# Optimization experiments

Measured on AMD Instinct MI355X. Metric: run time of the kernel, lower is better.

Reference implementation:

```python
import jax, jax.numpy as jnp
import numpy as np

IN_FEATURES = 4096
OUT_FEATURES = 8192
LUT_SIZE = 65536  # 256 * 256 two-level codebook


def setup_inputs() -> dict:
    key = jax.random.key(0)
    k_x, k_b, k_f, k_s, k_l = jax.random.split(key, 5)
    x = jax.random.normal(k_x, (2, 256, IN_FEATURES), dtype=jnp.float32)
    base_idx = jax.random.randint(k_b, (OUT_FEATURES, IN_FEATURES), 0, 256, dtype=jnp.int32)
    fine_idx = jax.random.randint(k_f, (OUT_FEATURES, IN_FEATURES), 0, 256, dtype=jnp.int32)
    scale = jax.random.uniform(k_s, (OUT_FEATURES, 1), dtype=jnp.float32)
    lut = jax.random.normal(k_l, (LUT_SIZE,), dtype=jnp.float32)
    return {"x": x, "base_idx": base_idx, "fine_idx": fine_idx, "scale": scale, "lut": lut}


def reference(x, base_idx, fine_idx, scale, lut):
    # Two-level LUT dequant: combined 16-bit index = base*256 + fine
    combined_idx = base_idx * 256 + fine_idx              # [out, in] int32
    weights = lut[combined_idx] * scale                   # [out, in] fp32, per-row scale
    # F.linear(x, weights) == x @ weights.T
    return jnp.einsum('bsi,oi->bso', x, weights)
```

## Files before the change

kernel.cpp:

```cpp
#include <hip/hip_runtime.h>

typedef unsigned short ushort_t;
typedef unsigned int   uint32;
typedef __attribute__((ext_vector_type(8)))  short short8;
typedef __attribute__((ext_vector_type(4)))  float floatx4;
typedef __attribute__((ext_vector_type(16))) float floatx16;
typedef __attribute__((ext_vector_type(4)))  int   intx4;
typedef __attribute__((ext_vector_type(4)))  float fltx4;

#define IN_F   4096
#define OUT_F  8192
#define M_TOT  512

__device__ __forceinline__ ushort_t f2bf(float f) {
    uint32 u = __builtin_bit_cast(uint32, f);
    u += 0x7FFFu + ((u >> 16) & 1u);
    return (ushort_t)(u >> 16);
}
__device__ __forceinline__ uint32 pack2bf(float a, float b) {
    return (uint32)f2bf(a) | ((uint32)f2bf(b) << 16);
}

__global__ void cvt_x_kernel(const float* __restrict__ x, ushort_t* __restrict__ xb) {
    const int g  = blockIdx.x * 256 + threadIdx.x;
    const int r  = g >> 9;
    const int k0 = (g & 511) * 8;
    float4 v0 = *(const float4*)(x + (size_t)r * IN_F + k0);
    float4 v1 = *(const float4*)(x + (size_t)r * IN_F + k0 + 4);
    short8 s;
    s[0] = (short)f2bf(v0.x); s[1] = (short)f2bf(v0.y);
    s[2] = (short)f2bf(v0.z); s[3] = (short)f2bf(v0.w);
    s[4] = (short)f2bf(v1.x); s[5] = (short)f2bf(v1.y);
    s[6] = (short)f2bf(v1.z); s[7] = (short)f2bf(v1.w);
    const int mt = r >> 5;
    const int kt = k0 >> 4;
    ushort_t* dst = xb + ((size_t)(mt * 256 + kt) * 32 + (r & 31)) * 16 + (k0 & 15);
    *(short8*)dst = s;
}

#define LGKM_BARRIER()                                          \
    asm volatile("s_waitcnt lgkmcnt(0)" ::: "memory");          \
    __builtin_amdgcn_sched_barrier(0);                          \
    __builtin_amdgcn_s_barrier();

__global__ __launch_bounds__(1024, 4)
void fused_kernel(const ushort_t* __restrict__ xb, const int* __restrict__ base_idx,
                  const int* __restrict__ fine_idx, const float* __restrict__ lut,
                  const float* __restrict__ scale, float* __restrict__ out)
{
    __shared__ ushort_t sh_lut[65536];
    __shared__ ushort_t sh_w[2][32 * 128];

    const int tid  = threadIdx.x;
    const int nblk = blockIdx.x;

    for (int i = tid * 4; i < 65536; i += 4096) {
        fltx4 v = __builtin_nontemporal_load((const fltx4*)(lut + i));
        *(uint32*)&sh_lut[i]     = pack2bf(v.x, v.y);
        *(uint32*)&sh_lut[i + 2] = pack2bf(v.z, v.w);
    }

    const int colr = tid >> 5;
    const int kq   = (tid & 31) * 4;
    const intx4* bp = (const intx4*)(base_idx + (size_t)(nblk * 32 + colr) * IN_F + kq);
    const intx4* fp = (const intx4*)(fine_idx + (size_t)(nblk * 32 + colr) * IN_F + kq);

    const int woff = colr * 128 + (((kq >> 3) ^ (colr & 7)) << 3) + (kq & 7);

    const int lane = tid & 63;
    const int wave = tid >> 6;
    const int l31  = lane & 31;
    const int lhi  = lane >> 5;
    const int rx8  = l31 & 7;

    const ushort_t* abase = xb + (size_t)wave * 256 * 512 + l31 * 16 + lhi * 8;

    intx4 ib0 = __builtin_nontemporal_load(bp);
    intx4 if0 = __builtin_nontemporal_load(fp);
    intx4 Ib  = __builtin_nontemporal_load(bp + 32);
    intx4 If  = __builtin_nontemporal_load(fp + 32);
    intx4 Nb  = __builtin_nontemporal_load(bp + 64);
    intx4 Nf  = __builtin_nontemporal_load(fp + 64);

    short8 aA[8], aB[8];
#pragma unroll
    for (int i = 0; i < 8; ++i)
        aA[i] = *(const short8*)(abase + (size_t)i * 512);

    LGKM_BARRIER();

    {
        uint32 w0 = (uint32)sh_lut[(ib0.x << 8) + if0.x]
                  | ((uint32)sh_lut[(ib0.y << 8) + if0.y] << 16);
        uint32 w1 = (uint32)sh_lut[(ib0.z << 8) + if0.z]
                  | ((uint32)sh_lut[(ib0.w << 8) + if0.w] << 16);
        uint2 wv; wv.x = w0; wv.y = w1;
        *(uint2*)&sh_w[0][woff] = wv;
    }

    LGKM_BARRIER();

    floatx16 acc = {0.f,0.f,0.f,0.f,0.f,0.f,0.f,0.f,0.f,0.f,0.f,0.f,0.f,0.f,0.f,0.f};

#define GBODY(T, AX, AY)                                                       \
    {                                                                          \
        const int cur = (T) & 1;                                               \
        const int tl  = ((T) + 3 < 32) ? (T) + 3 : 31;                         \
        intx4 Tb = __builtin_nontemporal_load(bp + tl * 32);                   \
        intx4 Tf = __builtin_nontemporal_load(fp + tl * 32);                   \
        if ((T) + 1 < 32) {                                                    \
            _Pragma("unroll")                                                  \
            for (int i = 0; i < 8; ++i)                                        \
                AY[i] = *(const short8*)(abase + (size_t)(((T) + 1) * 8 + i) * 512); \
        }                                                                      \
        const ushort_t* wb = sh_w[cur];                                        \
        __builtin_amdgcn_s_setprio(1);                                         \
        _Pragma("unroll")                                                      \
        for (int i = 0; i < 8; ++i) {                                          \
            short8 bfr = *(const short8*)&wb[l31 * 128 + (((2 * i + lhi) ^ rx8) << 3)]; \
            acc = __builtin_amdgcn_mfma_f32_32x32x16_bf16(AX[i], bfr, acc, 0, 0, 0);    \
        }                                                                      \
        __builtin_amdgcn_s_setprio(0);                                         \
        if ((T) < 31) {                                                        \
            uint32 w0 = (uint32)sh_lut[(Ib.x << 8) + If.x]                     \
                      | ((uint32)sh_lut[(Ib.y << 8) + If.y] << 16);            \
            uint32 w1 = (uint32)sh_lut[(Ib.z << 8) + If.z]                     \
                      | ((uint32)sh_lut[(Ib.w << 8) + If.w] << 16);            \
            uint2 wv; wv.x = w0; wv.y = w1;                                    \
            *(uint2*)&sh_w[cur ^ 1][woff] = wv;                                \
            Ib = Nb; If = Nf; Nb = Tb; Nf = Tf;                                \
        }                                                                      \
        LGKM_BARRIER();                                                        \
    }

    for (int t = 0; t < 32; t += 2) {
        GBODY(t, aA, aB)
        GBODY(t + 1, aB, aA)
    }
#undef GBODY

    const float sc = scale[nblk * 32 + l31];
    float* op = out + (size_t)(nblk * 32 + l31);
    const int rbase = wave * 32 + 4 * lhi;
#pragma unroll
    for (int reg = 0; reg < 16; ++reg) {
        const int row = rbase + (reg & 3) + 8 * (reg >> 2);
        op[(size_t)row * OUT_F] = acc[reg] * sc;
    }
}

#define NB  32
#define FBK 128
#define WS  136
#define NITER (IN_F / FBK)
__global__ __launch_bounds__(1024, 4)
void ghost_kernel(const float* __restrict__ xf,
                  const int* __restrict__ base_idx, const int* __restrict__ fine_idx,
                  const float* __restrict__ scale, const float* __restrict__ lut,
                  float* __restrict__ out)
{
    __shared__ ushort_t sh_lut[65536];
    __shared__ ushort_t sh_w[2][NB * WS];
    const int tid = threadIdx.x;
    const int n0  = blockIdx.x * NB;
    for (int i = tid * 4; i < 65536; i += 1024 * 4) {
        float4 v = *(const float4*)(lut + i);
        sh_lut[i + 0] = f2bf(v.x); sh_lut[i + 1] = f2bf(v.y);
        sh_lut[i + 2] = f2bf(v.z); sh_lut[i + 3] = f2bf(v.w);
    }
    const int sn  = tid >> 5;
    const int skq = (tid & 31) * 4;
    const int* bp = base_idx + (size_t)(n0 + sn) * IN_F + skq;
    const int* fp = fine_idx + (size_t)(n0 + sn) * IN_F + skq;
    __syncthreads();
    int4 pb = *(const int4*)(bp);
    int4 pf = *(const int4*)(fp);
    {
        uint32 w0 = (uint32)sh_lut[(pb.x << 8) + pf.x] | ((uint32)sh_lut[(pb.y << 8) + pf.y] << 16);
        uint32 w1 = (uint32)sh_lut[(pb.z << 8) + pf.z] | ((uint32)sh_lut[(pb.w << 8) + pf.w] << 16);
        uint2 wv; wv.x = w0; wv.y = w1;
        *(uint2*)&sh_w[0][sn * WS + skq] = wv;
    }
    pb = *(const int4*)(bp + FBK);
    pf = *(const int4*)(fp + FBK);
    __syncthreads();
    const int lane = tid & 63;
    const int wave = tid >> 6;
    const int l16  = lane & 15;
    const int quad = lane >> 4;
    floatx4 acc[2][2];
    const floatx4 zero = {0.f, 0.f, 0.f, 0.f};
    acc[0][0] = zero; acc[0][1] = zero; acc[1][0] = zero; acc[1][1] = zero;
    const int mrow = wave * 32 + l16;
    const float* xrowf = xf + (size_t)mrow * IN_F + quad * 8;
    for (int t = 0; t < NITER; ++t) {
        const int k0 = t * FBK;
        {
            uint32 w0 = (uint32)sh_lut[(pb.x << 8) + pf.x] | ((uint32)sh_lut[(pb.y << 8) + pf.y] << 16);
            uint32 w1 = (uint32)sh_lut[(pb.z << 8) + pf.z] | ((uint32)sh_lut[(pb.w << 8) + pf.w] << 16);
            uint2 wv; wv.x = w0; wv.y = w1;
            *(uint2*)&sh_w[(t + 1) & 1][sn * WS + skq] = wv;
        }
        {
            const int kk = (t + 2 < NITER ? t + 2 : NITER - 1) * FBK;
            pb = *(const int4*)(bp + kk);
            pf = *(const int4*)(fp + kk);
        }
        const ushort_t* wb = sh_w[t & 1];
#pragma unroll
        for (int ks = 0; ks < 4; ++ks) {
            const int kk = k0 + ks * 32;
            short8 b0 = *(const short8*)&wb[l16        * WS + ks * 32 + quad * 8];
            short8 b1 = *(const short8*)&wb[(16 + l16) * WS + ks * 32 + quad * 8];
            short8 a0, a1;
            const float* p0 = xrowf + kk;
            const float* p1 = xrowf + (size_t)16 * IN_F + kk;
            float4 u0 = *(const float4*)p0, u1 = *(const float4*)(p0 + 4);
            float4 v0 = *(const float4*)p1, v1 = *(const float4*)(p1 + 4);
            a0[0] = (short)f2bf(u0.x); a0[1] = (short)f2bf(u0.y);
            a0[2] = (short)f2bf(u0.z); a0[3] = (short)f2bf(u0.w);
            a0[4] = (short)f2bf(u1.x); a0[5] = (short)f2bf(u1.y);
            a0[6] = (short)f2bf(u1.z); a0[7] = (short)f2bf(u1.w);
            a1[0] = (short)f2bf(v0.x); a1[1] = (short)f2bf(v0.y);
            a1[2] = (short)f2bf(v0.z); a1[3] = (short)f2bf(v0.w);
            a1[4] = (short)f2bf(v1.x); a1[5] = (short)f2bf(v1.y);
            a1[6] = (short)f2bf(v1.z); a1[7] = (short)f2bf(v1.w);
            acc[0][0] = __builtin_amdgcn_mfma_f32_16x16x32_bf16(a0, b0, acc[0][0], 0, 0, 0);
            acc[0][1] = __builtin_amdgcn_mfma_f32_16x16x32_bf16(a0, b1, acc[0][1], 0, 0, 0);
            acc[1][0] = __builtin_amdgcn_mfma_f32_16x16x32_bf16(a1, b0, acc[1][0], 0, 0, 0);
            acc[1][1] = __builtin_amdgcn_mfma_f32_16x16x32_bf16(a1, b1, acc[1][1], 0, 0, 0);
        }
        __syncthreads();
    }
#pragma unroll
    for (int nf = 0; nf < 2; ++nf) {
        const int col = n0 + nf * 16 + l16;
        const float sc = scale[col];
#pragma unroll
        for (int f = 0; f < 2; ++f) {
            const int r0 = wave * 32 + f * 16 + quad * 4;
#pragma unroll
            for (int r = 0; r < 4; ++r) {
                out[(size_t)(r0 + r) * OUT_F + col] = acc[f][nf][r] * sc;
            }
        }
    }
}

extern "C" void kernel_launch(void* const* d_in, const int* in_sizes, int n_in,
                              void* d_out, int out_size, void* d_ws, size_t ws_size,
                              hipStream_t stream) {
    const float* x      = (const float*)d_in[0];
    const int*   bidx   = (const int*)d_in[1];
    const int*   fidx   = (const int*)d_in[2];
    const float* scale  = (const float*)d_in[3];
    const float* lut    = (const float*)d_in[4];
    float*       out    = (float*)d_out;

    const size_t xb_bytes = (size_t)M_TOT * IN_F * sizeof(ushort_t);

    if (ws_size >= xb_bytes) {
        ushort_t* xbuf = (ushort_t*)d_ws;
        cvt_x_kernel<<<1024, 256, 0, stream>>>(x, xbuf);
        fused_kernel<<<256, 1024, 0, stream>>>(xbuf, bidx, fidx, lut, scale, out);
    } else {
        ghost_kernel<<<OUT_F / NB, 1024, 0, stream>>>(x, bidx, fidx, scale, lut, out);
    }
}
```

Measured before the change: 328.5 us.

## Triple-buffer dequantized weight tiles and drop per-step LDS wait before barrier

The shared weight tile buffer grows from two to three slots, and the index prefetch distance increases by one step. Each step now writes the tile two steps ahead. The main loop is unrolled by six with fixed buffer indices. The explicit lgkmcnt(0) wait before each barrier is removed, so outstanding LDS reads and writes can overlap the barrier and the next step's MFMAs. In exchange, LDS use rises to about 152KB and the kernel relies on implicit ordering of LDS operations for correctness.

```diff
diff --git a/kernel.cpp b/kernel.cpp
--- a/kernel.cpp
+++ b/kernel.cpp
@@ -38,18 +38,13 @@
     *(short8*)dst = s;
 }
 
-#define LGKM_BARRIER()                                          \
-    asm volatile("s_waitcnt lgkmcnt(0)" ::: "memory");          \
-    __builtin_amdgcn_sched_barrier(0);                          \
-    __builtin_amdgcn_s_barrier();
-
 __global__ __launch_bounds__(1024, 4)
 void fused_kernel(const ushort_t* __restrict__ xb, const int* __restrict__ base_idx,
                   const int* __restrict__ fine_idx, const float* __restrict__ lut,
                   const float* __restrict__ scale, float* __restrict__ out)
 {
     __shared__ ushort_t sh_lut[65536];
-    __shared__ ushort_t sh_w[2][32 * 128];
+    __shared__ ushort_t sh_w[3][32 * 128];
 
     const int tid  = threadIdx.x;
     const int nblk = blockIdx.x;
@@ -75,45 +70,59 @@
 
     const ushort_t* abase = xb + (size_t)wave * 256 * 512 + l31 * 16 + lhi * 8;
 
-    intx4 ib0 = __builtin_nontemporal_load(bp);
-    intx4 if0 = __builtin_nontemporal_load(fp);
-    intx4 Ib  = __builtin_nontemporal_load(bp + 32);
-    intx4 If  = __builtin_nontemporal_load(fp + 32);
-    intx4 Nb  = __builtin_nontemporal_load(bp + 64);
-    intx4 Nf  = __builtin_nontemporal_load(fp + 64);
+    intx4 i0b = __builtin_nontemporal_load(bp);
+    intx4 i0f = __builtin_nontemporal_load(fp);
+    intx4 i1b = __builtin_nontemporal_load(bp + 32);
+    intx4 i1f = __builtin_nontemporal_load(fp + 32);
+    intx4 Ib  = __builtin_nontemporal_load(bp + 64);
+    intx4 If  = __builtin_nontemporal_load(fp + 64);
+    intx4 Nb  = __builtin_nontemporal_load(bp + 96);
+    intx4 Nf  = __builtin_nontemporal_load(fp + 96);
+    intx4 Pb = {0, 0, 0, 0}, Pf = {0, 0, 0, 0};
 
     short8 aA[8], aB[8];
 #pragma unroll
     for (int i = 0; i < 8; ++i)
         aA[i] = *(const short8*)(abase + (size_t)i * 512);
 
-    LGKM_BARRIER();
+    asm volatile("s_waitcnt lgkmcnt(0)" ::: "memory");
+    __builtin_amdgcn_sched_barrier(0);
+    __builtin_amdgcn_s_barrier();
 
     {
-        uint32 w0 = (uint32)sh_lut[(ib0.x << 8) + if0.x]
-                  | ((uint32)sh_lut[(ib0.y << 8) + if0.y] << 16);
-        uint32 w1 = (uint32)sh_lut[(ib0.z << 8) + if0.z]
-                  | ((uint32)sh_lut[(ib0.w << 8) + if0.w] << 16);
+        uint32 w0 = (uint32)sh_lut[(i0b.x << 8) + i0f.x]
+                  | ((uint32)sh_lut[(i0b.y << 8) + i0f.y] << 16);
+        uint32 w1 = (uint32)sh_lut[(i0b.z << 8) + i0f.z]
+                  | ((uint32)sh_lut[(i0b.w << 8) + i0f.w] << 16);
         uint2 wv; wv.x = w0; wv.y = w1;
         *(uint2*)&sh_w[0][woff] = wv;
-    }
-
-    LGKM_BARRIER();
+        w0 = (uint32)sh_lut[(i1b.x << 8) + i1f.x]
+           | ((uint32)sh_lut[(i1b.y << 8) + i1f.y] << 16);
+        w1 = (uint32)sh_lut[(i1b.z << 8) + i1f.z]
+           | ((uint32)sh_lut[(i1b.w << 8) + i1f.w] << 16);
+        wv.x = w0; wv.y = w1;
+        *(uint2*)&sh_w[1][woff] = wv;
+    }
+
+    asm volatile("s_waitcnt lgkmcnt(0)" ::: "memory");
+    __builtin_amdgcn_sched_barrier(0);
+    __builtin_amdgcn_s_barrier();
 
     floatx16 acc = {0.f,0.f,0.f,0.f,0.f,0.f,0.f,0.f,0.f,0.f,0.f,0.f,0.f,0.f,0.f,0.f};
 
-#define GBODY(T, AX, AY)                                                       \
+#define GBODY(K, AX, AY, CUR, WD)                                              \
     {                                                                          \
-        const int cur = (T) & 1;                                               \
-        const int tl  = ((T) + 3 < 32) ? (T) + 3 : 31;                         \
-        intx4 Tb = __builtin_nontemporal_load(bp + tl * 32);                   \
-        intx4 Tf = __builtin_nontemporal_load(fp + tl * 32);                   \
-        if ((T) + 1 < 32) {                                                    \
+        const int T = t + (K);                                                 \
+        if (T + 4 < 32) {                                                      \
+            Pb = __builtin_nontemporal_load(bp + (T + 4) * 32);                \
+            Pf = __builtin_nontemporal_load(fp + (T + 4) * 32);                \
+        }                                                                      \
+        if (T + 1 < 32) {                                                      \
             _Pragma("unroll")                                                  \
             for (int i = 0; i < 8; ++i)                                        \
-                AY[i] = *(const short8*)(abase + (size_t)(((T) + 1) * 8 + i) * 512); \
-        }                                                                      \
-        const ushort_t* wb = sh_w[cur];                                        \
+                AY[i] = *(const short8*)(abase + (size_t)((T + 1) * 8 + i) * 512); \
+        }                                                                      \
+        const ushort_t* wb = sh_w[CUR];                                        \
         __builtin_amdgcn_s_setprio(1);                                         \
         _Pragma("unroll")                                                      \
         for (int i = 0; i < 8; ++i) {                                          \
@@ -121,22 +130,30 @@
             acc = __builtin_amdgcn_mfma_f32_32x32x16_bf16(AX[i], bfr, acc, 0, 0, 0);    \
         }                                                                      \
         __builtin_amdgcn_s_setprio(0);                                         \
-        if ((T) < 31) {                                                        \
+        if (T + 2 < 32) {                                                      \
             uint32 w0 = (uint32)sh_lut[(Ib.x << 8) + If.x]                     \
                       | ((uint32)sh_lut[(Ib.y << 8) + If.y] << 16);            \
             uint32 w1 = (uint32)sh_lut[(Ib.z << 8) + If.z]                     \
                       | ((uint32)sh_lut[(Ib.w << 8) + If.w] << 16);            \
             uint2 wv; wv.x = w0; wv.y = w1;                                    \
-            *(uint2*)&sh_w[cur ^ 1][woff] = wv;                                \
-            Ib = Nb; If = Nf; Nb = Tb; Nf = Tf;                                \
-        }                                                                      \
-        LGKM_BARRIER();                                                        \
-    }
-
-    for (int t = 0; t < 32; t += 2) {
-        GBODY(t, aA, aB)
-        GBODY(t + 1, aB, aA)
-    }
+            *(uint2*)&sh_w[WD][woff] = wv;                                     \
+            Ib = Nb; If = Nf; Nb = Pb; Nf = Pf;                                \
+        }                                                                      \
+        __builtin_amdgcn_sched_barrier(0);                                     \
+        __builtin_amdgcn_s_barrier();                                          \
+    }
+
+    int t = 0;
+    for (; t < 30; t += 6) {
+        GBODY(0, aA, aB, 0, 2)
+        GBODY(1, aB, aA, 1, 0)
+        GBODY(2, aA, aB, 2, 1)
+        GBODY(3, aB, aA, 0, 2)
+        GBODY(4, aA, aB, 1, 0)
+        GBODY(5, aB, aA, 2, 1)
+    }
+    GBODY(0, aA, aB, 0, 2)
+    GBODY(1, aB, aA, 1, 0)
 #undef GBODY
 
     const float sc = scale[nblk * 32 + l31];
```

Measured after the change: 327.3 us. About the same (-0.4%).
